# Kernel tuning notes

Measured on AMD Instinct MI355X. Metric: run time of the kernel, lower is better.

The kernel has to match this reference:

```python
import jax, jax.numpy as jnp
import numpy as np
from jax import lax

N_STEPS = 4  # matches init n_steps


def setup_inputs() -> dict:
    key = jax.random.key(0)
    ks = jax.random.split(key, 12)
    B, N, D, E = 32, 256, 512, 4
    prop_state = jax.random.normal(ks[0], (B, N, D), dtype=jnp.float32)
    edges = (jax.random.uniform(ks[1], (B, N, N * E * 2)) < 0.02).astype(jnp.float32)
    s = 0.02  # matches weight.data.normal_(0.0, 0.02)
    return {
        "prop_state": prop_state,
        "edges": edges,
        "W_in": jax.random.normal(ks[2], (E, D, D), dtype=jnp.float32) * s,
        "b_in": jnp.zeros((E, D), jnp.float32),
        "W_out": jax.random.normal(ks[3], (E, D, D), dtype=jnp.float32) * s,
        "b_out": jnp.zeros((E, D), jnp.float32),
        "W_r": jax.random.normal(ks[4], (3 * D, D), dtype=jnp.float32) * s,
        "b_r": jnp.zeros((D,), jnp.float32),
        "W_z": jax.random.normal(ks[5], (3 * D, D), dtype=jnp.float32) * s,
        "b_z": jnp.zeros((D,), jnp.float32),
        "W_h": jax.random.normal(ks[6], (3 * D, D), dtype=jnp.float32) * s,
        "b_h": jnp.zeros((D,), jnp.float32),
        "W_bridge_h": jax.random.normal(ks[7], (D, D), dtype=jnp.float32) * s,
        "b_bridge_h": jnp.zeros((D,), jnp.float32),
        "W_bridge_c": jax.random.normal(ks[8], (D, D), dtype=jnp.float32) * s,
        "b_bridge_c": jnp.zeros((D,), jnp.float32),
    }


def reference(prop_state, edges, W_in, b_in, W_out, b_out,
              W_r, b_r, W_z, b_z, W_h, b_h,
              W_bridge_h, b_bridge_h, W_bridge_c, b_bridge_c):
    B, N, D = prop_state.shape
    E = W_in.shape[0]
    edges_in = edges[:, :, : N * E]   # [B, N, N*E]
    edges_out = edges[:, :, N * E:]   # [B, N, N*E]

    def step(state, _):
        # per-edge-type linear transforms, edge-type-major layout [B, E*N, D]
        ins = (jnp.einsum('bnd,edh->bend', state, W_in)
               + b_in[None, :, None, :]).reshape(B, E * N, D)
        outs = (jnp.einsum('bnd,edh->bend', state, W_out)
                + b_out[None, :, None, :]).reshape(B, E * N, D)
        a_in = jnp.einsum('bnm,bmd->bnd', edges_in, ins)    # bmm aggregation
        a_out = jnp.einsum('bnm,bmd->bnd', edges_out, outs)
        a = jnp.concatenate([a_in, a_out, state], axis=2)   # [B, N, 3D]
        r = jax.nn.sigmoid(a @ W_r + b_r)
        z = jax.nn.sigmoid(a @ W_z + b_z)
        joined = jnp.concatenate([a_in, a_out, r * state], axis=2)
        h_hat = jax.nn.leaky_relu(joined @ W_h + b_h)        # slope 0.01 as torch
        return (1.0 - z) * state + z * h_hat, None

    state, _ = lax.scan(step, prop_state, None, length=N_STEPS)

    # bridge (bridge_extra_node=False path): mean over dim 0, 4 stacked copies
    join = state.mean(axis=0)                     # [N, D]
    js = jnp.broadcast_to(join, (4,) + join.shape)  # [4, N, D]
    h = jax.nn.relu(js @ W_bridge_h + b_bridge_h)
    c = jax.nn.relu(js @ W_bridge_c + b_bridge_c)
    return state, h, c
```

## Files before the change

kernel.cpp:

```cpp
#include <hip/hip_runtime.h>
#include <math.h>


typedef __bf16 bf16_t;
typedef __bf16 bf16x8 __attribute__((ext_vector_type(8)));
typedef __bf16 bf16x4_t __attribute__((ext_vector_type(4)));
typedef float f32x4 __attribute__((ext_vector_type(4)));

__device__ __forceinline__ void stage_lds16(const bf16_t* __restrict__ g, int ld,
                                            bf16_t* __restrict__ s) {
  int wave = threadIdx.x >> 6;
  int lane = threadIdx.x & 63;
  int rsub = lane >> 2;
  int k0 = (lane & 3) << 3;
#pragma unroll
  for (int i = 0; i < 2; ++i) {
    int c = wave + (i << 2);
    const bf16_t* gp = g + (size_t)((c << 4) + rsub) * ld + k0;
    __builtin_amdgcn_global_load_lds(
        (const __attribute__((address_space(1))) void*)gp,
        (__attribute__((address_space(3))) void*)(s + (c << 9)), 16, 0, 0);
  }
}

__device__ __forceinline__ void stage_lds16_64(const bf16_t* __restrict__ g, int ld,
                                               bf16_t* __restrict__ s) {
  int wave = threadIdx.x >> 6;
  int lane = threadIdx.x & 63;
  int rsub = lane >> 2;
  int k0 = (lane & 3) << 3;
  const bf16_t* gp = g + (size_t)((wave << 4) + rsub) * ld + k0;
  __builtin_amdgcn_global_load_lds(
      (const __attribute__((address_space(1))) void*)gp,
      (__attribute__((address_space(3))) void*)(s + (wave << 9)), 16, 0, 0);
}

__device__ __forceinline__ bf16x8 frag(const bf16_t* s, int r, int koff) {
  return *reinterpret_cast<const bf16x8*>(s + (r << 5) + koff);
}


__global__ __launch_bounds__(256) void k_build_idx(const float* __restrict__ edges,
                                                   unsigned short* __restrict__ nbr,
                                                   uchar4* __restrict__ cnt4) {
  int wid = threadIdx.x >> 6, lane = threadIdx.x & 63;
  int W = blockIdx.x * 4 + wid;
  int b = W >> 9, io = (W >> 8) & 1, n = W & 255;
  const float* p = edges + (size_t)(b * 256 + n) * 2048 + io * 1024;
  unsigned short* list = nbr + (size_t)W * 64;
  int base = 0;
  int ends[4];
#pragma unroll
  for (int e = 0; e < 4; ++e) {
#pragma unroll
    for (int ch = 0; ch < 4; ++ch) {
      int c = e * 256 + ch * 64 + lane;
      float v = p[c];
      unsigned long long mask = __ballot(v != 0.0f);
      int before = __popcll(mask & ((1ull << lane) - 1ull));
      if (v != 0.0f && (base + before) < 64) list[base + before] = (unsigned short)c;
      base += __popcll(mask);
    }
    ends[e] = base < 64 ? base : 64;
  }
  if (lane == 0)
    cnt4[W] = make_uchar4((unsigned char)ends[0], (unsigned char)ends[1],
                          (unsigned char)ends[2], (unsigned char)ends[3]);
}

__global__ __launch_bounds__(256) void k_rowsum(const float* __restrict__ W,
                                                float* __restrict__ wsum, int nrows) {
  int wid = threadIdx.x >> 6, lane = threadIdx.x & 63;
  int row = blockIdx.x * 4 + wid;
  if (row >= nrows) return;
  const float4* p = reinterpret_cast<const float4*>(W + (size_t)row * 512);
  float s = 0.f;
#pragma unroll
  for (int i = 0; i < 2; ++i) {
    float4 v = p[lane + i * 64];
    s += v.x + v.y + v.z + v.w;
  }
#pragma unroll
  for (int off = 32; off > 0; off >>= 1) s += __shfl_down(s, off, 64);
  if (lane == 0) wsum[row] = s;
}

__global__ __launch_bounds__(256) void k_transpose_cvt(const float* __restrict__ src,
                                                       bf16_t* __restrict__ dst,
                                                       int K, int N) {
  __shared__ float tile[32][33];
  int z = blockIdx.z;
  src += (size_t)z * K * N;
  dst += (size_t)z * K * N;
  int tx = threadIdx.x & 31, ty = threadIdx.x >> 5;
  int n0 = blockIdx.x * 32, k0 = blockIdx.y * 32;
#pragma unroll
  for (int i = 0; i < 4; ++i)
    tile[ty + i * 8][tx] = src[(size_t)(k0 + ty + i * 8) * N + n0 + tx];
  __syncthreads();
#pragma unroll
  for (int i = 0; i < 4; ++i)
    dst[(size_t)(n0 + ty + i * 8) * K + k0 + tx] = (bf16_t)tile[tx][ty + i * 8];
}

__global__ __launch_bounds__(256) void k_transpose_into(const float* __restrict__ src,
                                                        bf16_t* __restrict__ dst,
                                                        int Ksrc, int ld) {
  __shared__ float tile[32][33];
  int tx = threadIdx.x & 31, ty = threadIdx.x >> 5;
  int n0 = blockIdx.x * 32, k0 = blockIdx.y * 32;
  if (k0 >= Ksrc) {
#pragma unroll
    for (int i = 0; i < 4; ++i)
      dst[(size_t)(n0 + ty + i * 8) * ld + k0 + tx] = (bf16_t)0.0f;
    return;
  }
#pragma unroll
  for (int i = 0; i < 4; ++i)
    tile[ty + i * 8][tx] = src[(size_t)(k0 + ty + i * 8) * 512 + n0 + tx];
  __syncthreads();
#pragma unroll
  for (int i = 0; i < 4; ++i)
    dst[(size_t)(n0 + ty + i * 8) * ld + k0 + tx] = (bf16_t)tile[tx][ty + i * 8];
}

__global__ __launch_bounds__(256) void k_state_init(const float* __restrict__ src,
                                                    float* __restrict__ dst_f32,
                                                    bf16_t* __restrict__ dst_b, int n4) {
  int i = blockIdx.x * 256 + threadIdx.x;
  if (i < n4) {
    float4 v = reinterpret_cast<const float4*>(src)[i];
    reinterpret_cast<float4*>(dst_f32)[i] = v;
    bf16x4_t o;
    o[0] = (bf16_t)v.x; o[1] = (bf16_t)v.y; o[2] = (bf16_t)v.z; o[3] = (bf16_t)v.w;
    *reinterpret_cast<bf16x4_t*>(dst_b + i * 4) = o;
  }
}

__global__ __launch_bounds__(256) void k_agg_sparse(const unsigned short* __restrict__ nbr,
                                                    const uchar4* __restrict__ cnt4,
                                                    const bf16_t* __restrict__ state_b,
                                                    const float* __restrict__ wsum_in,
                                                    const float* __restrict__ wsum_out,
                                                    const float* __restrict__ b_in,
                                                    const float* __restrict__ b_out,
                                                    bf16_t* __restrict__ ain_b,
                                                    bf16_t* __restrict__ aout_b) {
  int wid = threadIdx.x >> 6, lane = threadIdx.x & 63;
  int W = blockIdx.x * 4 + wid;
  int b = W >> 9, io = (W >> 8) & 1, n = W & 255;
  const float* wsel = io ? wsum_out : wsum_in;
  const float* bsel = io ? b_out : b_in;
  int d0 = lane << 3;
  float w[4][8], bi[4][8];
#pragma unroll
  for (int e = 0; e < 4; ++e) {
#pragma unroll
    for (int t = 0; t < 8; t += 4) {
      float4 v = *reinterpret_cast<const float4*>(wsel + e * 512 + d0 + t);
      w[e][t] = v.x; w[e][t + 1] = v.y; w[e][t + 2] = v.z; w[e][t + 3] = v.w;
      float4 u = *reinterpret_cast<const float4*>(bsel + e * 512 + d0 + t);
      bi[e][t] = u.x; bi[e][t + 1] = u.y; bi[e][t + 2] = u.z; bi[e][t + 3] = u.w;
    }
  }
  int mycode = nbr[(size_t)W * 64 + lane];
  uchar4 ce = cnt4[W];
  float acc[8];
#pragma unroll
  for (int t = 0; t < 8; ++t) acc[t] = 0.f;
  const bf16_t* Sb = state_b + ((size_t)b << 17) + d0;
  int start = 0;
#pragma unroll
  for (int e = 0; e < 4; ++e) {
    int end = (e == 0) ? ce.x : (e == 1) ? ce.y : (e == 2) ? ce.z : ce.w;
    float fc = (float)(end - start);
#pragma unroll
    for (int t = 0; t < 8; ++t) acc[t] += fc * bi[e][t];
    for (int j = start; j < end; ++j) {
      int c = __shfl(mycode, j, 64);
      int m = c & 255;
      bf16x8 s = *reinterpret_cast<const bf16x8*>(Sb + ((size_t)m << 9));
#pragma unroll
      for (int t = 0; t < 8; ++t) acc[t] += (float)s[t] * w[e][t];
    }
    start = end;
  }
  bf16x8 o;
#pragma unroll
  for (int t = 0; t < 8; ++t) o[t] = (bf16_t)acc[t];
  bf16_t* dst = io ? aout_b : ain_b;
  *reinterpret_cast<bf16x8*>(dst + (size_t)(b * 256 + n) * 512 + d0) = o;
}

__global__ __launch_bounds__(256, 4) void k_gates(const bf16_t* __restrict__ ain_b,
                                                  const bf16_t* __restrict__ aout_b,
                                                  const bf16_t* __restrict__ state_row_b,
                                                  const bf16_t* __restrict__ Wall_t,
                                                  const float* __restrict__ b_r,
                                                  const float* __restrict__ b_z,
                                                  const float* __restrict__ b_h,
                                                  bf16_t* __restrict__ rs_b,
                                                  bf16_t* __restrict__ zb_b,
                                                  bf16_t* __restrict__ hp_b) {
  __shared__ __align__(16) char smem[32768];
  bf16_t* As0 = (bf16_t*)smem;
  bf16_t* Bs0 = (bf16_t*)(smem + 16384);
  float* tr = (float*)smem;
  int mt = blockIdx.x, nt = blockIdx.y;
  int gm0 = mt * 128, gn0 = nt * 128;
  int lane = threadIdx.x & 63, wid = threadIdx.x >> 6;
  int wr = wid >> 1, wc = wid & 1;
  int l15 = lane & 15, q = lane >> 4, koff = q << 3;
  int nkt = (nt < 8) ? 48 : 32;
  f32x4 acc[4][4];
#pragma unroll
  for (int i = 0; i < 4; ++i)
#pragma unroll
    for (int j = 0; j < 4; ++j) acc[i][j] = f32x4{0.f, 0.f, 0.f, 0.f};

  auto stageAB = [&](int buf, int kt) {
    int blk = kt >> 4, kk = (kt & 15) << 5;
    const bf16_t* gA = (blk == 0 ? ain_b : blk == 1 ? aout_b : state_row_b)
                       + (size_t)gm0 * 512 + kk;
    stage_lds16(gA, 512, As0 + buf * 4096);
    stage_lds16(Wall_t + (size_t)gn0 * 1536 + (kt << 5), 1536, Bs0 + buf * 4096);
  };

  stageAB(0, 0);
  __syncthreads();
  int cur = 0;
  for (int kt = 0; kt < nkt; ++kt) {
    if (kt + 1 < nkt) stageAB(cur ^ 1, kt + 1);
    bf16x8 af[4], bfr[4];
#pragma unroll
    for (int i = 0; i < 4; ++i) af[i] = frag(As0 + cur * 4096, wr * 64 + i * 16 + l15, koff);
#pragma unroll
    for (int j = 0; j < 4; ++j) bfr[j] = frag(Bs0 + cur * 4096, wc * 64 + j * 16 + l15, koff);
#pragma unroll
    for (int i = 0; i < 4; ++i)
#pragma unroll
      for (int j = 0; j < 4; ++j)
        acc[i][j] = __builtin_amdgcn_mfma_f32_16x16x32_bf16(af[i], bfr[j], acc[i][j], 0, 0, 0);
    __syncthreads();
    cur ^= 1;
  }

  int region = nt >> 2;
  int cn0 = gn0 - region * 512;
  const float* bias = region == 0 ? b_r : region == 1 ? b_z : b_h;
#pragma unroll
  for (int p = 0; p < 4; ++p) {
    __syncthreads();
    if (wc == (p >> 1)) {
      int j0 = (p & 1) << 1;
#pragma unroll
      for (int jj = 0; jj < 2; ++jj) {
        int j = j0 + jj;
        int c = j * 16 + l15 - ((p & 1) << 5);
#pragma unroll
        for (int i = 0; i < 4; ++i)
#pragma unroll
          for (int rr = 0; rr < 4; ++rr) {
            int row = wr * 64 + i * 16 + q * 4 + rr;
            tr[row * 36 + c] = acc[i][j][rr];
          }
      }
    }
    __syncthreads();
#pragma unroll
    for (int s = 0; s < 16; ++s) {
      int e = threadIdx.x + (s << 8);
      int row = e >> 5, c = e & 31;
      int col = cn0 + (p << 5) + c;
      size_t idx = (size_t)(gm0 + row) * 512 + col;
      float x = tr[row * 36 + c] + bias[col];
      if (region == 0) {
        float rg = 1.0f / (1.0f + __expf(-x));
        rs_b[idx] = (bf16_t)(rg * (float)state_row_b[idx]);
      } else if (region == 1) {
        zb_b[idx] = (bf16_t)(1.0f / (1.0f + __expf(-x)));
      } else {
        hp_b[idx] = (bf16_t)x;
      }
    }
  }
}

__global__ __launch_bounds__(256, 4) void k_gru(const bf16_t* __restrict__ rs_b,
                                                const bf16_t* __restrict__ Whb_t,
                                                const bf16_t* __restrict__ hp_b,
                                                const bf16_t* __restrict__ zb_b,
                                                float* __restrict__ state_f32,
                                                bf16_t* __restrict__ state_row_b) {
  __shared__ __align__(16) char smem[24576];
  bf16_t* As0 = (bf16_t*)smem;
  bf16_t* Bs0 = (bf16_t*)(smem + 8192);
  float* tr = (float*)smem;
  int mt = blockIdx.x, nt = blockIdx.y;
  int gm0 = mt * 64, gn0 = nt * 128;
  int lane = threadIdx.x & 63, wid = threadIdx.x >> 6;
  int wr = wid >> 1, wc = wid & 1;
  int l15 = lane & 15, q = lane >> 4, koff = q << 3;
  f32x4 acc[2][4];
#pragma unroll
  for (int i = 0; i < 2; ++i)
#pragma unroll
    for (int j = 0; j < 4; ++j) acc[i][j] = f32x4{0.f, 0.f, 0.f, 0.f};

  auto stageAB = [&](int buf, int kt) {
    stage_lds16_64(rs_b + (size_t)gm0 * 512 + (kt << 5), 512, As0 + buf * 2048);
    stage_lds16(Whb_t + (size_t)gn0 * 512 + (kt << 5), 512, Bs0 + buf * 4096);
  };

  stageAB(0, 0);
  __syncthreads();
  int cur = 0;
  for (int kt = 0; kt < 16; ++kt) {
    if (kt + 1 < 16) stageAB(cur ^ 1, kt + 1);
    bf16x8 af[2], bfr[4];
#pragma unroll
    for (int i = 0; i < 2; ++i) af[i] = frag(As0 + cur * 2048, wr * 32 + i * 16 + l15, koff);
#pragma unroll
    for (int j = 0; j < 4; ++j) bfr[j] = frag(Bs0 + cur * 4096, wc * 64 + j * 16 + l15, koff);
#pragma unroll
    for (int i = 0; i < 2; ++i)
#pragma unroll
      for (int j = 0; j < 4; ++j)
        acc[i][j] = __builtin_amdgcn_mfma_f32_16x16x32_bf16(af[i], bfr[j], acc[i][j], 0, 0, 0);
    __syncthreads();
    cur ^= 1;
  }

#pragma unroll
  for (int p = 0; p < 4; ++p) {
    __syncthreads();
    if (wc == (p >> 1)) {
      int j0 = (p & 1) << 1;
#pragma unroll
      for (int jj = 0; jj < 2; ++jj) {
        int j = j0 + jj;
        int c = j * 16 + l15 - ((p & 1) << 5);
#pragma unroll
        for (int i = 0; i < 2; ++i)
#pragma unroll
          for (int rr = 0; rr < 4; ++rr) {
            int row = wr * 32 + i * 16 + q * 4 + rr;
            tr[row * 36 + c] = acc[i][j][rr];
          }
      }
    }
    __syncthreads();
#pragma unroll
    for (int s = 0; s < 8; ++s) {
      int e = threadIdx.x + (s << 8);
      int row = e >> 5, c = e & 31;
      int col = gn0 + (p << 5) + c;
      size_t idx = (size_t)(gm0 + row) * 512 + col;
      float x = tr[row * 36 + c] + (float)hp_b[idx];
      float hh = x > 0.0f ? x : 0.01f * x;
      float z = (float)zb_b[idx];
      float so = state_f32[idx];
      float sn = (1.0f - z) * so + z * hh;
      state_f32[idx] = sn;
      state_row_b[idx] = (bf16_t)sn;
    }
  }
}


__global__ __launch_bounds__(256) void k_join(const float* __restrict__ state_f32,
                                              bf16_t* __restrict__ join_b) {
  int idx = blockIdx.x * 256 + threadIdx.x;
  float s = 0.f;
#pragma unroll
  for (int b = 0; b < 32; ++b) s += state_f32[(size_t)b * 131072 + idx];
  join_b[idx] = (bf16_t)(s * (1.0f / 32.0f));
}

__global__ __launch_bounds__(256) void k_bridge(const bf16_t* __restrict__ join_b,
                                                const bf16_t* __restrict__ Wbh_t,
                                                const bf16_t* __restrict__ Wbc_t,
                                                const float* __restrict__ b_bh,
                                                const float* __restrict__ b_bc,
                                                float* __restrict__ out_h,
                                                float* __restrict__ out_c) {
  __shared__ bf16_t As[2][4096];
  __shared__ bf16_t Bs[2][4096];
  int mt = blockIdx.x, nt = blockIdx.y, hc = blockIdx.z;
  const bf16_t* Wt = hc ? Wbc_t : Wbh_t;
  const float* bias = hc ? b_bc : b_bh;
  float* dst = hc ? out_c : out_h;
  int gm0 = mt * 128, gn0 = nt * 128;
  int lane = threadIdx.x & 63, wid = threadIdx.x >> 6;
  int wr = wid >> 1, wc = wid & 1;
  int l15 = lane & 15, koff = (lane >> 4) << 3;
  f32x4 acc[4][4];
#pragma unroll
  for (int i = 0; i < 4; ++i)
#pragma unroll
    for (int j = 0; j < 4; ++j) acc[i][j] = f32x4{0.f, 0.f, 0.f, 0.f};
  auto stageAB = [&](int buf, int kt) {
    stage_lds16(join_b + (size_t)gm0 * 512 + (kt << 5), 512, As[buf]);
    stage_lds16(Wt + (size_t)gn0 * 512 + (kt << 5), 512, Bs[buf]);
  };
  stageAB(0, 0);
  __syncthreads();
  int cur = 0;
  for (int kt = 0; kt < 16; ++kt) {
    if (kt + 1 < 16) stageAB(cur ^ 1, kt + 1);
    bf16x8 af[4], bfr[4];
#pragma unroll
    for (int i = 0; i < 4; ++i) af[i] = frag(As[cur], wr * 64 + i * 16 + l15, koff);
#pragma unroll
    for (int j = 0; j < 4; ++j) bfr[j] = frag(Bs[cur], wc * 64 + j * 16 + l15, koff);
#pragma unroll
    for (int i = 0; i < 4; ++i)
#pragma unroll
      for (int j = 0; j < 4; ++j)
        acc[i][j] = __builtin_amdgcn_mfma_f32_16x16x32_bf16(af[i], bfr[j], acc[i][j], 0, 0, 0);
    __syncthreads();
    cur ^= 1;
  }
  int lr0 = (lane >> 4) << 2;
#pragma unroll
  for (int j = 0; j < 4; ++j) {
    int col = gn0 + wc * 64 + j * 16 + l15;
    float bv = bias[col];
#pragma unroll
    for (int i = 0; i < 4; ++i) {
#pragma unroll
      for (int r = 0; r < 4; ++r) {
        int row = gm0 + wr * 64 + i * 16 + lr0 + r;
        float v = acc[i][j][r] + bv;
        v = v > 0.f ? v : 0.f;
#pragma unroll
        for (int rep = 0; rep < 4; ++rep)
          dst[(size_t)rep * 131072 + (size_t)row * 512 + col] = v;
      }
    }
  }
}


extern "C" void kernel_launch(void* const* d_in, const int* in_sizes, int n_in,
                              void* d_out, int out_size, void* d_ws, size_t ws_size,
                              hipStream_t stream) {
  const float* prop_state = (const float*)d_in[0];
  const float* edges = (const float*)d_in[1];
  const float* W_in = (const float*)d_in[2];
  const float* b_in = (const float*)d_in[3];
  const float* W_out = (const float*)d_in[4];
  const float* b_out = (const float*)d_in[5];
  const float* W_r = (const float*)d_in[6];
  const float* b_r = (const float*)d_in[7];
  const float* W_z = (const float*)d_in[8];
  const float* b_z = (const float*)d_in[9];
  const float* W_h = (const float*)d_in[10];
  const float* b_h = (const float*)d_in[11];
  const float* W_bh = (const float*)d_in[12];
  const float* b_bh = (const float*)d_in[13];
  const float* W_bc = (const float*)d_in[14];
  const float* b_bc = (const float*)d_in[15];

  float* out_state = (float*)d_out;
  float* out_h = out_state + 4194304;
  float* out_c = out_h + 524288;

  char* ws = (char*)d_ws;
  size_t off = 0;
  auto alloc = [&](size_t bytes) -> void* {
    void* p = ws + off;
    off += (bytes + 255) & ~(size_t)255;
    return p;
  };
  unsigned short* nbr = (unsigned short*)alloc(16384ull * 64 * 2);
  uchar4* cnt4   = (uchar4*)alloc(16384ull * 4);
  float* wsum_in  = (float*)alloc(2048ull * 4);
  float* wsum_out = (float*)alloc(2048ull * 4);
  bf16_t* Wall_t = (bf16_t*)alloc(1536ull * 1536 * 2);
  bf16_t* Whb_t  = (bf16_t*)alloc(512ull * 512 * 2);
  bf16_t* Wbh_t  = (bf16_t*)alloc(512ull * 512 * 2);
  bf16_t* Wbc_t  = (bf16_t*)alloc(512ull * 512 * 2);
  bf16_t* state_b = (bf16_t*)alloc(4194304ull * 2);
  bf16_t* ain_b  = (bf16_t*)alloc(4194304ull * 2);
  bf16_t* aout_b = (bf16_t*)alloc(4194304ull * 2);
  bf16_t* rs_b   = (bf16_t*)alloc(4194304ull * 2);
  bf16_t* zb_b   = (bf16_t*)alloc(4194304ull * 2);
  bf16_t* hp_b   = (bf16_t*)alloc(4194304ull * 2);
  bf16_t* join_b = (bf16_t*)alloc(131072ull * 2);
  if (off > ws_size) return;

  k_build_idx<<<4096, 256, 0, stream>>>(edges, nbr, cnt4);
  k_rowsum<<<512, 256, 0, stream>>>(W_in, wsum_in, 2048);
  k_rowsum<<<512, 256, 0, stream>>>(W_out, wsum_out, 2048);
  k_transpose_into<<<dim3(16, 48), 256, 0, stream>>>(W_r, Wall_t, 1536, 1536);
  k_transpose_into<<<dim3(16, 48), 256, 0, stream>>>(W_z, Wall_t + 512 * 1536, 1536, 1536);
  k_transpose_into<<<dim3(16, 48), 256, 0, stream>>>(W_h, Wall_t + 1024 * 1536, 1024, 1536);
  k_transpose_into<<<dim3(16, 16), 256, 0, stream>>>(W_h + 1024 * 512, Whb_t, 512, 512);
  k_transpose_cvt<<<dim3(16, 16, 1), 256, 0, stream>>>(W_bh, Wbh_t, 512, 512);
  k_transpose_cvt<<<dim3(16, 16, 1), 256, 0, stream>>>(W_bc, Wbc_t, 512, 512);
  k_state_init<<<4096, 256, 0, stream>>>(prop_state, out_state, state_b, 1048576);

  for (int step = 0; step < 4; ++step) {
    k_agg_sparse<<<4096, 256, 0, stream>>>(nbr, cnt4, state_b, wsum_in, wsum_out,
                                           b_in, b_out, ain_b, aout_b);
    k_gates<<<dim3(64, 12), 256, 0, stream>>>(ain_b, aout_b, state_b, Wall_t,
                                              b_r, b_z, b_h, rs_b, zb_b, hp_b);
    k_gru<<<dim3(128, 4), 256, 0, stream>>>(rs_b, Whb_t, hp_b, zb_b,
                                            out_state, state_b);
  }

  k_join<<<512, 256, 0, stream>>>(out_state, join_b);
  k_bridge<<<dim3(2, 4, 2), 256, 0, stream>>>(join_b, Wbh_t, Wbc_t, b_bh, b_bc, out_h, out_c);
}
```

Before: 560.2 us.

## Triple-buffer LDS in gate and GRU GEMMs and merge weight prep launches

The k_gates and k_gru GEMM loops move from double to triple LDS buffering. Tile loads are issued two k-steps ahead, and explicit s_waitcnt vmcnt counts with raw s_barrier calls replace __syncthreads, so global->LDS copies overlap more of the MFMA work. The six weight transpose and convert launches are merged into two batched launches to cut launch overhead. The larger LDS footprint (48KB and 36KB per block) may lower occupancy, and the hand-tuned vmcnt values must match the number of outstanding loads to stay correct.

Result: no change. 565.3 us (+0.9%).

```diff
diff --git a/kernel.cpp b/kernel.cpp
--- a/kernel.cpp
+++ b/kernel.cpp
@@ -39,6 +39,9 @@
   return *reinterpret_cast<const bf16x8*>(s + (r << 5) + koff);
 }
 
+#define SBAR() __builtin_amdgcn_s_barrier()
+#define SCHED0() __builtin_amdgcn_sched_barrier(0)
+
 
 __global__ __launch_bounds__(256) void k_build_idx(const float* __restrict__ edges,
                                                    unsigned short* __restrict__ nbr,
@@ -85,34 +88,21 @@
   if (lane == 0) wsum[row] = s;
 }
 
-__global__ __launch_bounds__(256) void k_transpose_cvt(const float* __restrict__ src,
-                                                       bf16_t* __restrict__ dst,
-                                                       int K, int N) {
+__global__ __launch_bounds__(256) void k_prep_wall(const float* __restrict__ Wr,
+                                                   const float* __restrict__ Wz,
+                                                   const float* __restrict__ Wh,
+                                                   bf16_t* __restrict__ dst) {
   __shared__ float tile[32][33];
   int z = blockIdx.z;
-  src += (size_t)z * K * N;
-  dst += (size_t)z * K * N;
-  int tx = threadIdx.x & 31, ty = threadIdx.x >> 5;
-  int n0 = blockIdx.x * 32, k0 = blockIdx.y * 32;
-#pragma unroll
-  for (int i = 0; i < 4; ++i)
-    tile[ty + i * 8][tx] = src[(size_t)(k0 + ty + i * 8) * N + n0 + tx];
-  __syncthreads();
-#pragma unroll
-  for (int i = 0; i < 4; ++i)
-    dst[(size_t)(n0 + ty + i * 8) * K + k0 + tx] = (bf16_t)tile[tx][ty + i * 8];
-}
-
-__global__ __launch_bounds__(256) void k_transpose_into(const float* __restrict__ src,
-                                                        bf16_t* __restrict__ dst,
-                                                        int Ksrc, int ld) {
-  __shared__ float tile[32][33];
+  const float* src = z == 0 ? Wr : z == 1 ? Wz : Wh;
+  int Ksrc = z == 2 ? 1024 : 1536;
+  bf16_t* d = dst + (size_t)(z * 512) * 1536;
   int tx = threadIdx.x & 31, ty = threadIdx.x >> 5;
   int n0 = blockIdx.x * 32, k0 = blockIdx.y * 32;
   if (k0 >= Ksrc) {
 #pragma unroll
     for (int i = 0; i < 4; ++i)
-      dst[(size_t)(n0 + ty + i * 8) * ld + k0 + tx] = (bf16_t)0.0f;
+      d[(size_t)(n0 + ty + i * 8) * 1536 + k0 + tx] = (bf16_t)0.0f;
     return;
   }
 #pragma unroll
@@ -121,7 +111,28 @@
   __syncthreads();
 #pragma unroll
   for (int i = 0; i < 4; ++i)
-    dst[(size_t)(n0 + ty + i * 8) * ld + k0 + tx] = (bf16_t)tile[tx][ty + i * 8];
+    d[(size_t)(n0 + ty + i * 8) * 1536 + k0 + tx] = (bf16_t)tile[tx][ty + i * 8];
+}
+
+__global__ __launch_bounds__(256) void k_prep_small(const float* __restrict__ Whb_src,
+                                                    const float* __restrict__ Wbh_src,
+                                                    const float* __restrict__ Wbc_src,
+                                                    bf16_t* __restrict__ Whb_t,
+                                                    bf16_t* __restrict__ Wbh_t,
+                                                    bf16_t* __restrict__ Wbc_t) {
+  __shared__ float tile[32][33];
+  int z = blockIdx.z;
+  const float* src = z == 0 ? Whb_src : z == 1 ? Wbh_src : Wbc_src;
+  bf16_t* dst = z == 0 ? Whb_t : z == 1 ? Wbh_t : Wbc_t;
+  int tx = threadIdx.x & 31, ty = threadIdx.x >> 5;
+  int n0 = blockIdx.x * 32, k0 = blockIdx.y * 32;
+#pragma unroll
+  for (int i = 0; i < 4; ++i)
+    tile[ty + i * 8][tx] = src[(size_t)(k0 + ty + i * 8) * 512 + n0 + tx];
+  __syncthreads();
+#pragma unroll
+  for (int i = 0; i < 4; ++i)
+    dst[(size_t)(n0 + ty + i * 8) * 512 + k0 + tx] = (bf16_t)tile[tx][ty + i * 8];
 }
 
 __global__ __launch_bounds__(256) void k_state_init(const float* __restrict__ src,
@@ -202,9 +213,7 @@
                                                   bf16_t* __restrict__ rs_b,
                                                   bf16_t* __restrict__ zb_b,
                                                   bf16_t* __restrict__ hp_b) {
-  __shared__ __align__(16) char smem[32768];
-  bf16_t* As0 = (bf16_t*)smem;
-  bf16_t* Bs0 = (bf16_t*)(smem + 16384);
+  __shared__ __align__(16) char smem[49152];
   float* tr = (float*)smem;
   int mt = blockIdx.x, nt = blockIdx.y;
   int gm0 = mt * 128, gn0 = nt * 128;
@@ -222,27 +231,40 @@
     int blk = kt >> 4, kk = (kt & 15) << 5;
     const bf16_t* gA = (blk == 0 ? ain_b : blk == 1 ? aout_b : state_row_b)
                        + (size_t)gm0 * 512 + kk;
-    stage_lds16(gA, 512, As0 + buf * 4096);
-    stage_lds16(Wall_t + (size_t)gn0 * 1536 + (kt << 5), 1536, Bs0 + buf * 4096);
+    bf16_t* base = (bf16_t*)(smem + buf * 16384);
+    stage_lds16(gA, 512, base);
+    stage_lds16(Wall_t + (size_t)gn0 * 1536 + (kt << 5), 1536, base + 4096);
   };
 
   stageAB(0, 0);
-  __syncthreads();
-  int cur = 0;
+  stageAB(1, 1);
+  asm volatile("s_waitcnt vmcnt(4)" ::: "memory");
+  SCHED0(); SBAR(); SCHED0();
+
+  int b0 = 0, b1 = 1, b2 = 2;
   for (int kt = 0; kt < nkt; ++kt) {
-    if (kt + 1 < nkt) stageAB(cur ^ 1, kt + 1);
+    const bf16_t* As = (const bf16_t*)(smem + b0 * 16384);
+    const bf16_t* Bs = As + 4096;
     bf16x8 af[4], bfr[4];
 #pragma unroll
-    for (int i = 0; i < 4; ++i) af[i] = frag(As0 + cur * 4096, wr * 64 + i * 16 + l15, koff);
-#pragma unroll
-    for (int j = 0; j < 4; ++j) bfr[j] = frag(Bs0 + cur * 4096, wc * 64 + j * 16 + l15, koff);
+    for (int i = 0; i < 4; ++i) af[i] = frag(As, wr * 64 + i * 16 + l15, koff);
+#pragma unroll
+    for (int j = 0; j < 4; ++j) bfr[j] = frag(Bs, wc * 64 + j * 16 + l15, koff);
 #pragma unroll
     for (int i = 0; i < 4; ++i)
 #pragma unroll
       for (int j = 0; j < 4; ++j)
         acc[i][j] = __builtin_amdgcn_mfma_f32_16x16x32_bf16(af[i], bfr[j], acc[i][j], 0, 0, 0);
-    __syncthreads();
-    cur ^= 1;
+    SCHED0(); SBAR(); SCHED0();
+    if (kt + 2 < nkt) {
+      stageAB(b2, kt + 2);
+      asm volatile("s_waitcnt vmcnt(4)" ::: "memory");
+      SCHED0(); SBAR(); SCHED0();
+    } else if (kt + 1 < nkt) {
+      asm volatile("s_waitcnt vmcnt(0)" ::: "memory");
+      SCHED0(); SBAR(); SCHED0();
+    }
+    int t = b0; b0 = b1; b1 = b2; b2 = t;
   }
 
   int region = nt >> 2;
@@ -292,9 +314,7 @@
                                                 const bf16_t* __restrict__ zb_b,
                                                 float* __restrict__ state_f32,
                                                 bf16_t* __restrict__ state_row_b) {
-  __shared__ __align__(16) char smem[24576];
-  bf16_t* As0 = (bf16_t*)smem;
-  bf16_t* Bs0 = (bf16_t*)(smem + 8192);
+  __shared__ __align__(16) char smem[36864];
   float* tr = (float*)smem;
   int mt = blockIdx.x, nt = blockIdx.y;
   int gm0 = mt * 64, gn0 = nt * 128;
@@ -308,27 +328,40 @@
     for (int j = 0; j < 4; ++j) acc[i][j] = f32x4{0.f, 0.f, 0.f, 0.f};
 
   auto stageAB = [&](int buf, int kt) {
-    stage_lds16_64(rs_b + (size_t)gm0 * 512 + (kt << 5), 512, As0 + buf * 2048);
-    stage_lds16(Whb_t + (size_t)gn0 * 512 + (kt << 5), 512, Bs0 + buf * 4096);
+    bf16_t* base = (bf16_t*)(smem + buf * 12288);
+    stage_lds16_64(rs_b + (size_t)gm0 * 512 + (kt << 5), 512, base);
+    stage_lds16(Whb_t + (size_t)gn0 * 512 + (kt << 5), 512, base + 2048);
   };
 
   stageAB(0, 0);
-  __syncthreads();
-  int cur = 0;
+  stageAB(1, 1);
+  asm volatile("s_waitcnt vmcnt(3)" ::: "memory");
+  SCHED0(); SBAR(); SCHED0();
+
+  int b0 = 0, b1 = 1, b2 = 2;
   for (int kt = 0; kt < 16; ++kt) {
-    if (kt + 1 < 16) stageAB(cur ^ 1, kt + 1);
+    const bf16_t* As = (const bf16_t*)(smem + b0 * 12288);
+    const bf16_t* Bs = As + 2048;
     bf16x8 af[2], bfr[4];
 #pragma unroll
-    for (int i = 0; i < 2; ++i) af[i] = frag(As0 + cur * 2048, wr * 32 + i * 16 + l15, koff);
-#pragma unroll
-    for (int j = 0; j < 4; ++j) bfr[j] = frag(Bs0 + cur * 4096, wc * 64 + j * 16 + l15, koff);
+    for (int i = 0; i < 2; ++i) af[i] = frag(As, wr * 32 + i * 16 + l15, koff);
+#pragma unroll
+    for (int j = 0; j < 4; ++j) bfr[j] = frag(Bs, wc * 64 + j * 16 + l15, koff);
 #pragma unroll
     for (int i = 0; i < 2; ++i)
 #pragma unroll
       for (int j = 0; j < 4; ++j)
         acc[i][j] = __builtin_amdgcn_mfma_f32_16x16x32_bf16(af[i], bfr[j], acc[i][j], 0, 0, 0);
-    __syncthreads();
-    cur ^= 1;
+    SCHED0(); SBAR(); SCHED0();
+    if (kt + 2 < 16) {
+      stageAB(b2, kt + 2);
+      asm volatile("s_waitcnt vmcnt(3)" ::: "memory");
+      SCHED0(); SBAR(); SCHED0();
+    } else if (kt + 1 < 16) {
+      asm volatile("s_waitcnt vmcnt(0)" ::: "memory");
+      SCHED0(); SBAR(); SCHED0();
+    }
+    int t = b0; b0 = b1; b1 = b2; b2 = t;
   }
 
 #pragma unroll
@@ -493,12 +526,9 @@
   k_build_idx<<<4096, 256, 0, stream>>>(edges, nbr, cnt4);
   k_rowsum<<<512, 256, 0, stream>>>(W_in, wsum_in, 2048);
   k_rowsum<<<512, 256, 0, stream>>>(W_out, wsum_out, 2048);
-  k_transpose_into<<<dim3(16, 48), 256, 0, stream>>>(W_r, Wall_t, 1536, 1536);
-  k_transpose_into<<<dim3(16, 48), 256, 0, stream>>>(W_z, Wall_t + 512 * 1536, 1536, 1536);
-  k_transpose_into<<<dim3(16, 48), 256, 0, stream>>>(W_h, Wall_t + 1024 * 1536, 1024, 1536);
-  k_transpose_into<<<dim3(16, 16), 256, 0, stream>>>(W_h + 1024 * 512, Whb_t, 512, 512);
-  k_transpose_cvt<<<dim3(16, 16, 1), 256, 0, stream>>>(W_bh, Wbh_t, 512, 512);
-  k_transpose_cvt<<<dim3(16, 16, 1), 256, 0, stream>>>(W_bc, Wbc_t, 512, 512);
+  k_prep_wall<<<dim3(16, 48, 3), 256, 0, stream>>>(W_r, W_z, W_h, Wall_t);
+  k_prep_small<<<dim3(16, 16, 3), 256, 0, stream>>>(W_h + 1024 * 512, W_bh, W_bc,
+                                                    Whb_t, Wbh_t, Wbc_t);
   k_state_init<<<4096, 256, 0, stream>>>(prop_state, out_state, state_b, 1048576);
 
   for (int step = 0; step < 4; ++step) {
```
